# Optimization experiments

Measured on AMD Instinct MI355X. Metric: run time of the kernel, lower is better.

Reference implementation:

```python
import jax, jax.numpy as jnp
import numpy as np

N, M = 8192, 1024  # n_frames, feature dim (input_size == output_size == 1024)
Q_SCALE = 0.06
DROP_P = 0.5


def setup_inputs() -> dict:
    key = jax.random.key(0)
    kx, kk, kq, kv, ko, ku = jax.random.split(key, 6)
    w_std = 0.02
    return {
        "x": jax.random.normal(kx, (N, M), dtype=jnp.float32),
        # nn.Linear stores weight as [out_features, in_features]
        "Wk": jax.random.normal(kk, (M, M), dtype=jnp.float32) * w_std,
        "Wq": jax.random.normal(kq, (M, M), dtype=jnp.float32) * w_std,
        "Wv": jax.random.normal(kv, (M, M), dtype=jnp.float32) * w_std,
        "Wo": jax.random.normal(ko, (M, M), dtype=jnp.float32) * w_std,
        # uniform noise for dropout mask on the [N, N] attention matrix
        "u": jax.random.uniform(ku, (N, N), dtype=jnp.float32),
    }


def reference(x, Wk, Wq, Wv, Wo, u):
    # projections (bias-free Linear: y = x @ W.T)
    K = x @ Wk.T                      # [N, M]
    Q = (x @ Wq.T) * Q_SCALE          # [N, M], Q *= 0.06
    V = x @ Wv.T                      # [N, M]
    logits = Q @ K.T                  # [N, N]
    attn = jax.nn.softmax(logits, axis=-1)
    # Dropout(p=0.5) in train mode: keep with prob 0.5, scale by 1/(1-p)=2
    keep = jnp.where(u >= DROP_P, jnp.float32(1.0 / (1.0 - DROP_P)), jnp.float32(0.0))
    w = attn * keep                   # [N, N]
    y = w @ V                         # [N, M]
    return y @ Wo.T                   # [N, M]
```

## Files before the change

kernel.cpp:

```cpp
#include <hip/hip_runtime.h>
#include <cstdint>
#include <cstddef>

#define NFRAMES 8192
#define MDIM    1024
#define Q_SCALE 0.06f

#define BK 64
#define BM2 256
#define BN2 256
#define BM 256
#define BN 128

typedef __bf16 bf16x8 __attribute__((ext_vector_type(8)));
typedef float  f32x4  __attribute__((ext_vector_type(4)));
typedef unsigned short us8 __attribute__((ext_vector_type(8)));

__device__ __forceinline__ unsigned short f2bf(float f) {
  union { float f; uint32_t u; } a; a.f = f;
  uint32_t u = a.u;
  u += 0x7FFFu + ((u >> 16) & 1u);
  return (unsigned short)(u >> 16);
}
__device__ __forceinline__ float bf2f(unsigned short h) {
  union { uint32_t u; float f; } a; a.u = ((uint32_t)h) << 16; return a.f;
}

__device__ __forceinline__ void async_ld16(const void* g, void* l) {
  __builtin_amdgcn_global_load_lds(
      (const __attribute__((address_space(1))) void*)(uintptr_t)g,
      (__attribute__((address_space(3))) void*)(uint32_t)(uintptr_t)l,
      16, 0, 0);
}

__device__ __forceinline__ void store_val(float* p, float v) { *p = v; }
__device__ __forceinline__ void store_val(unsigned short* p, float v) { *p = f2bf(v); }

template <typename OutT>
__global__ __launch_bounds__(512, 2) void gemm_8ph(
    const unsigned short* __restrict__ A, int lda,
    const unsigned short* __restrict__ B, int ldb,
    OutT* __restrict__ C, int ldc, long cz, int kChunk)
{
  __shared__ alignas(16) unsigned short As[2 * BM2 * BK];
  __shared__ alignas(16) unsigned short Bs[2 * BN2 * BK];

  const int tid  = threadIdx.x;
  const int wave = tid >> 6;
  const int lane = tid & 63;

  const int gX  = (int)gridDim.x;
  const int nwg = gX * (int)gridDim.y;
  int bx = (int)blockIdx.x, by = (int)blockIdx.y;
  if ((nwg & 7) == 0) {
    const int L  = by * gX + bx;
    const int qq = nwg >> 3;
    const int Ls = (L & 7) * qq + (L >> 3);
    bx = Ls % gX; by = Ls / gX;
  }

  const int m0 = by * BM2, n0 = bx * BN2;
  const int wm = (wave >> 2) * 128;
  const int wn = (wave & 3) * 64;
  const int fr = lane & 15, fq = lane >> 4;

  const int kOff = (int)blockIdx.z * kChunk;
  OutT* Cz = C + (size_t)blockIdx.z * cz;

  const int l8 = lane >> 3, l7 = lane & 7;
  const size_t ldaB = (size_t)lda * 2, ldbB = (size_t)ldb * 2;
  const char* aSrc = (const char*)A + (size_t)(m0 + wave * 8 + l8) * ldaB
                     + (size_t)kOff * 2 + ((l7 ^ l8) << 4);
  const char* bSrc = (const char*)B + (size_t)(n0 + wave * 8 + l8) * ldbB
                     + (size_t)kOff * 2 + ((l7 ^ l8) << 4);

  const int xorv = (fr & 7) << 4;
  const int c0 = (fq * 16) ^ xorv;
  const int c1 = (64 + fq * 16) ^ xorv;
  const char* aRd = (const char*)As + (wm + fr) * 128;
  const char* bRd = (const char*)Bs + (wn + fr) * 128;
  const char* aB0 = aRd;
  const char* aB1 = aRd + 32768;
  const char* bB0 = bRd;
  const char* bB1 = bRd + 32768;

  f32x4 acc[8][4] = {};
  const int NT = kChunk >> 6;
  const int NI = NT >> 1;

#define SA(b, h, t) do { \
  async_ld16(aSrc + (size_t)((h) * 128)      * ldaB + (size_t)(t) * 128, \
             As + (b) * 16384 + (h) * 8192 + wave * 512); \
  async_ld16(aSrc + (size_t)((h) * 128 + 64) * ldaB + (size_t)(t) * 128, \
             As + (b) * 16384 + (h) * 8192 + 4096 + wave * 512); \
} while (0)
#define SB(b, h, t) do { \
  async_ld16(bSrc + (size_t)((h) * 128)      * ldbB + (size_t)(t) * 128, \
             Bs + (b) * 16384 + (h) * 8192 + wave * 512); \
  async_ld16(bSrc + (size_t)((h) * 128 + 64) * ldbB + (size_t)(t) * 128, \
             Bs + (b) * 16384 + (h) * 8192 + 4096 + wave * 512); \
} while (0)

#define RD_A(dst, base, mh) do { \
  _Pragma("unroll") \
  for (int m_ = 0; m_ < 4; ++m_) { \
    dst[m_][0] = *(const bf16x8*)((base) + ((mh) * 4 + m_) * 2048 + c0); \
    dst[m_][1] = *(const bf16x8*)((base) + ((mh) * 4 + m_) * 2048 + c1); \
  } \
} while (0)
#define RD_B(dst, base, nh) do { \
  _Pragma("unroll") \
  for (int n_ = 0; n_ < 2; ++n_) { \
    dst[n_][0] = *(const bf16x8*)((base) + ((nh) * 2 + n_) * 2048 + c0); \
    dst[n_][1] = *(const bf16x8*)((base) + ((nh) * 2 + n_) * 2048 + c1); \
  } \
} while (0)

#define BARR() __builtin_amdgcn_s_barrier()
#define LGKM0() do { asm volatile("s_waitcnt lgkmcnt(0)" ::: "memory"); \
                     __builtin_amdgcn_sched_barrier(0); } while (0)
#define MM(mh, nh, af, bf) do { \
  __builtin_amdgcn_s_setprio(1); \
  _Pragma("unroll") \
  for (int kk_ = 0; kk_ < 2; ++kk_) \
  _Pragma("unroll") \
  for (int m_ = 0; m_ < 4; ++m_) \
  _Pragma("unroll") \
  for (int n_ = 0; n_ < 2; ++n_) \
    acc[(mh) * 4 + m_][(nh) * 2 + n_] = __builtin_amdgcn_mfma_f32_16x16x32_bf16( \
        af[m_][kk_], bf[n_][kk_], acc[(mh) * 4 + m_][(nh) * 2 + n_], 0, 0, 0); \
  __builtin_amdgcn_s_setprio(0); \
} while (0)

#define BODY(G, T1) do { \
  bf16x8 aF[4][2], bF0[2][2], bF1[2][2]; \
   \
  RD_A(aF, aB0, 0); RD_B(bF0, bB0, 0); \
  SA(1, 0, (T1)); \
  BARR(); LGKM0(); MM(0, 0, aF, bF0); BARR(); \
   \
  RD_B(bF1, bB0, 1); \
  SA(1, 1, (T1)); \
  BARR(); LGKM0(); MM(0, 1, aF, bF1); BARR(); \
   \
  RD_A(aF, aB0, 1); \
  if (G) SB(0, 0, (T1) + 1); \
  BARR(); LGKM0(); MM(1, 0, aF, bF0); BARR(); \
   \
  if (G) SB(0, 1, (T1) + 1); \
  BARR(); MM(1, 1, aF, bF1); \
  if (G) { asm volatile("s_waitcnt vmcnt(4)" ::: "memory"); } \
  else   { asm volatile("s_waitcnt vmcnt(0)" ::: "memory"); } \
  BARR(); __builtin_amdgcn_sched_barrier(0); \
   \
  RD_A(aF, aB1, 0); RD_B(bF0, bB1, 0); \
  if (G) SA(0, 0, (T1) + 1); \
  BARR(); LGKM0(); MM(0, 0, aF, bF0); BARR(); \
   \
  RD_B(bF1, bB1, 1); \
  if (G) SA(0, 1, (T1) + 1); \
  BARR(); LGKM0(); MM(0, 1, aF, bF1); BARR(); \
   \
  RD_A(aF, aB1, 1); \
  if (G) SB(1, 0, (T1) + 2); \
  BARR(); LGKM0(); MM(1, 0, aF, bF0); BARR(); \
   \
  if (G) SB(1, 1, (T1) + 2); \
  BARR(); MM(1, 1, aF, bF1); \
  if (G) { asm volatile("s_waitcnt vmcnt(4)" ::: "memory"); } \
  BARR(); __builtin_amdgcn_sched_barrier(0); \
} while (0)

  SA(0, 0, 0); SA(0, 1, 0);
  SB(0, 0, 0); SB(0, 1, 0);
  SB(1, 0, 1); SB(1, 1, 1);
  asm volatile("s_waitcnt vmcnt(4)" ::: "memory");
  BARR();
  __builtin_amdgcn_sched_barrier(0);

  for (int i = 0; i + 1 < NI; ++i) {
    BODY(true, 2 * i + 1);
  }
  BODY(false, NT - 1);

#undef SA
#undef SB
#undef RD_A
#undef RD_B
#undef BARR
#undef LGKM0
#undef MM
#undef BODY

#pragma unroll
  for (int mf = 0; mf < 8; ++mf)
#pragma unroll
    for (int nf = 0; nf < 4; ++nf)
#pragma unroll
      for (int r = 0; r < 4; ++r) {
        int row = m0 + wm + mf * 16 + fq * 4 + r;
        int col = n0 + wn + nf * 16 + fr;
        store_val(&Cz[(size_t)row * ldc + col], acc[mf][nf][r]);
      }
}

template <typename OutT>
__global__ __launch_bounds__(512, 2) void gemm_bt8(
    const unsigned short* __restrict__ A, int lda,
    const unsigned short* __restrict__ B, int ldb,
    OutT* __restrict__ C, int ldc, int K)
{
  __shared__ alignas(16) unsigned short As[3 * BM * BK];
  __shared__ alignas(16) unsigned short Bs[3 * BN * BK];

  const int tid  = threadIdx.x;
  const int wave = tid >> 6;
  const int lane = tid & 63;

  const int gX  = (int)gridDim.x;
  const int nwg = gX * (int)gridDim.y;
  const int L   = (int)blockIdx.y * gX + (int)blockIdx.x;
  const int qq  = nwg >> 3;
  const int Ls  = (L & 7) * qq + (L >> 3);
  const int bx  = Ls % gX, by = Ls / gX;

  const int m0 = by * BM, n0 = bx * BN;
  const int wm = (wave >> 1) * 64;
  const int wn = (wave & 1) * 64;
  const int fr = lane & 15, fq = lane >> 4;

  const int l8 = lane >> 3, l7 = lane & 7;
  const size_t ldaB = (size_t)lda * 2, ldbB = (size_t)ldb * 2;
  const char* aSrc = (const char*)A + (size_t)(m0 + wave * 8 + l8) * ldaB + ((l7 ^ l8) << 4);
  const char* bSrc = (const char*)B + (size_t)(n0 + wave * 8 + l8) * ldbB + ((l7 ^ l8) << 4);
  unsigned short* aDst = As + wave * 512;
  unsigned short* bDst = Bs + wave * 512;

  const int xorv = (fr & 7) << 4;
  const int cA0 = (fq * 16) ^ xorv;
  const int cA1 = (64 + fq * 16) ^ xorv;
  const char* aRd = (const char*)As + (wm + fr) * 128;
  const char* bRd = (const char*)Bs + (wn + fr) * 128;

  f32x4 acc[4][4] = {};
  const int NT = K >> 6;

#define STA(buf, s, t) async_ld16(aSrc + (size_t)((s) * 64) * ldaB + (size_t)(t) * 128, \
                                  aDst + (buf) * 16384 + (s) * 4096)
#define STB(buf, s, t) async_ld16(bSrc + (size_t)((s) * 64) * ldbB + (size_t)(t) * 128, \
                                  bDst + (buf) * 8192 + (s) * 4096)

  STA(0, 0, 0); STA(0, 1, 0); STA(0, 2, 0); STA(0, 3, 0); STB(0, 0, 0); STB(0, 1, 0);
  if (NT > 1) { STA(1, 0, 1); STA(1, 1, 1); STA(1, 2, 1); STA(1, 3, 1); STB(1, 0, 1); STB(1, 1, 1); }
  asm volatile("s_waitcnt vmcnt(6)" ::: "memory");
  __builtin_amdgcn_s_barrier();

  for (int t = 0; t < NT; ++t) {
    const int cur = t % 3;
    const int u   = t + 2;
    const int ub  = u % 3;
    const bool st = (u < NT);
    const char* aB = aRd + cur * 32768;
    const char* bB = bRd + cur * 16384;

    bf16x8 bh[4][2];
#pragma unroll
    for (int j = 0; j < 4; ++j) {
      bh[j][0] = *(const bf16x8*)(bB + j * 2048 + cA0);
      bh[j][1] = *(const bf16x8*)(bB + j * 2048 + cA1);
    }
    bf16x8 a0[2][2];
#pragma unroll
    for (int i = 0; i < 2; ++i) {
      a0[i][0] = *(const bf16x8*)(aB + i * 2048 + cA0);
      a0[i][1] = *(const bf16x8*)(aB + i * 2048 + cA1);
    }
    if (st) { STA(ub, 0, u); STA(ub, 1, u); STB(ub, 0, u); }
    __builtin_amdgcn_s_barrier();
    asm volatile("s_waitcnt lgkmcnt(0)" ::: "memory");
    __builtin_amdgcn_sched_barrier(0);
    __builtin_amdgcn_s_setprio(1);
#pragma unroll
    for (int kk = 0; kk < 2; ++kk)
#pragma unroll
      for (int i = 0; i < 2; ++i)
#pragma unroll
        for (int j = 0; j < 4; ++j)
          acc[i][j] = __builtin_amdgcn_mfma_f32_16x16x32_bf16(
              kk ? a0[i][1] : a0[i][0], kk ? bh[j][1] : bh[j][0], acc[i][j], 0, 0, 0);
    __builtin_amdgcn_s_setprio(0);
    __builtin_amdgcn_s_barrier();

    bf16x8 a1[2][2];
#pragma unroll
    for (int i = 0; i < 2; ++i) {
      a1[i][0] = *(const bf16x8*)(aB + (2 + i) * 2048 + cA0);
      a1[i][1] = *(const bf16x8*)(aB + (2 + i) * 2048 + cA1);
    }
    if (st) { STA(ub, 2, u); STA(ub, 3, u); STB(ub, 1, u); }
    if (st) { asm volatile("s_waitcnt vmcnt(6)" ::: "memory"); }
    else    { asm volatile("s_waitcnt vmcnt(0)" ::: "memory"); }
    __builtin_amdgcn_s_barrier();
    asm volatile("s_waitcnt lgkmcnt(0)" ::: "memory");
    __builtin_amdgcn_sched_barrier(0);
    __builtin_amdgcn_s_setprio(1);
#pragma unroll
    for (int kk = 0; kk < 2; ++kk)
#pragma unroll
      for (int i = 0; i < 2; ++i)
#pragma unroll
        for (int j = 0; j < 4; ++j)
          acc[2 + i][j] = __builtin_amdgcn_mfma_f32_16x16x32_bf16(
              kk ? a1[i][1] : a1[i][0], kk ? bh[j][1] : bh[j][0], acc[2 + i][j], 0, 0, 0);
    __builtin_amdgcn_s_setprio(0);
    __builtin_amdgcn_s_barrier();
  }
#undef STA
#undef STB

#pragma unroll
  for (int i = 0; i < 4; ++i)
#pragma unroll
    for (int j = 0; j < 4; ++j)
#pragma unroll
      for (int r = 0; r < 4; ++r) {
        int row = m0 + wm + i * 16 + fq * 4 + r;
        int col = n0 + wn + j * 16 + fr;
        store_val(&C[(size_t)row * ldc + col], acc[i][j][r]);
      }
}

__global__ __launch_bounds__(256) void softmax_dropout_kernel(
    const unsigned short* __restrict__ S, const float* __restrict__ U,
    unsigned short* __restrict__ P)
{
  const int row = blockIdx.x;
  const us8*   s8 = (const us8*)(S + (size_t)row * NFRAMES);
  const f32x4* u4 = (const f32x4*)(U + (size_t)row * NFRAMES);
  us8*         p8 = (us8*)(P + (size_t)row * NFRAMES);
  const int tid = threadIdx.x;
  const int lane = tid & 63, wave = tid >> 6;

  float v[32];
  float mx = -3.4e38f;
#pragma unroll
  for (int j = 0; j < 4; ++j) {
    us8 t = __builtin_nontemporal_load(s8 + j * 256 + tid);
#pragma unroll
    for (int e = 0; e < 8; ++e) {
      float f = bf2f(t[e]);
      v[j * 8 + e] = f;
      mx = fmaxf(mx, f);
    }
  }
#pragma unroll
  for (int o = 32; o > 0; o >>= 1) mx = fmaxf(mx, __shfl_xor(mx, o));
  __shared__ float redm[4];
  __shared__ float reds[4];
  if (lane == 0) redm[wave] = mx;
  __syncthreads();
  mx = fmaxf(fmaxf(redm[0], redm[1]), fmaxf(redm[2], redm[3]));

  float sum = 0.f;
#pragma unroll
  for (int i = 0; i < 32; ++i) { v[i] = __expf(v[i] - mx); sum += v[i]; }
#pragma unroll
  for (int o = 32; o > 0; o >>= 1) sum += __shfl_xor(sum, o);
  if (lane == 0) reds[wave] = sum;
  __syncthreads();
  sum = reds[0] + reds[1] + reds[2] + reds[3];
  float inv = 1.0f / sum;

#pragma unroll
  for (int j = 0; j < 4; ++j) {
    f32x4 ua = __builtin_nontemporal_load(u4 + (j * 256 + tid) * 2);
    f32x4 ub = __builtin_nontemporal_load(u4 + (j * 256 + tid) * 2 + 1);
    us8 o;
    o[0] = f2bf(v[j*8+0] * inv * (ua[0] >= 0.5f ? 2.0f : 0.0f));
    o[1] = f2bf(v[j*8+1] * inv * (ua[1] >= 0.5f ? 2.0f : 0.0f));
    o[2] = f2bf(v[j*8+2] * inv * (ua[2] >= 0.5f ? 2.0f : 0.0f));
    o[3] = f2bf(v[j*8+3] * inv * (ua[3] >= 0.5f ? 2.0f : 0.0f));
    o[4] = f2bf(v[j*8+4] * inv * (ub[0] >= 0.5f ? 2.0f : 0.0f));
    o[5] = f2bf(v[j*8+5] * inv * (ub[1] >= 0.5f ? 2.0f : 0.0f));
    o[6] = f2bf(v[j*8+6] * inv * (ub[2] >= 0.5f ? 2.0f : 0.0f));
    o[7] = f2bf(v[j*8+7] * inv * (ub[3] >= 0.5f ? 2.0f : 0.0f));
    p8[j * 256 + tid] = o;
  }
}

__device__ __forceinline__ void cvt4(const float* in, unsigned short* out, int i, float s) {
  float4 t = ((const float4*)in)[i];
  ushort4 o;
  o.x = f2bf(t.x * s); o.y = f2bf(t.y * s); o.z = f2bf(t.z * s); o.w = f2bf(t.w * s);
  ((ushort4*)out)[i] = o;
}

__global__ __launch_bounds__(256) void cvt_all(
    const float* __restrict__ x, const float* __restrict__ Wk,
    const float* __restrict__ Wq, const float* __restrict__ Wv,
    const float* __restrict__ Wo,
    unsigned short* __restrict__ xb, unsigned short* __restrict__ wkq,
    unsigned short* __restrict__ wvb, unsigned short* __restrict__ wob)
{
  int i = blockIdx.x * 256 + threadIdx.x;
  const int XSZ = (NFRAMES * MDIM) / 4;
  const int WSZ = (MDIM * MDIM) / 4;
  if (i < XSZ) { cvt4(x, xb, i, 1.0f); return; }
  i -= XSZ;
  if (i < WSZ) { cvt4(Wk, wkq, i, 1.0f); return; }
  i -= WSZ;
  if (i < WSZ) { cvt4(Wq, wkq + MDIM * MDIM, i, Q_SCALE); return; }
  i -= WSZ;
  if (i < WSZ) { cvt4(Wv, wvb, i, 1.0f); return; }
  i -= WSZ;
  if (i < WSZ) { cvt4(Wo, wob, i, 1.0f); return; }
}

__global__ __launch_bounds__(256) void reduce2_bf16(
    const float* __restrict__ Yp, long zs,
    unsigned short* __restrict__ out, int n4)
{
  int i = blockIdx.x * 256 + threadIdx.x;
  if (i < n4) {
    f32x4 a = __builtin_nontemporal_load((const f32x4*)Yp + i);
    f32x4 b = __builtin_nontemporal_load((const f32x4*)(Yp + zs) + i);
    ushort4 o;
    o.x = f2bf(a[0] + b[0]);
    o.y = f2bf(a[1] + b[1]);
    o.z = f2bf(a[2] + b[2]);
    o.w = f2bf(a[3] + b[3]);
    ((ushort4*)out)[i] = o;
  }
}

extern "C" void kernel_launch(void* const* d_in, const int* in_sizes, int n_in,
                              void* d_out, int out_size, void* d_ws, size_t ws_size,
                              hipStream_t stream) {
  const float* x  = (const float*)d_in[0];
  const float* Wk = (const float*)d_in[1];
  const float* Wq = (const float*)d_in[2];
  const float* Wv = (const float*)d_in[3];
  const float* Wo = (const float*)d_in[4];
  const float* u  = (const float*)d_in[5];
  float* out = (float*)d_out;

  const int N = NFRAMES, M = MDIM;
  char* base = (char*)d_ws;
  size_t off = 0;
  auto alloc = [&](size_t bytes) -> void* {
    void* p = base + off; off += (bytes + 255) & ~(size_t)255; return p;
  };
  unsigned short* xb  = (unsigned short*)alloc((size_t)N * M * 2);
  unsigned short* wkq = (unsigned short*)alloc((size_t)2 * M * M * 2);
  unsigned short* wvb = (unsigned short*)alloc((size_t)M * M * 2);
  unsigned short* wob = (unsigned short*)alloc((size_t)M * M * 2);
  unsigned short* KQb = (unsigned short*)alloc((size_t)N * 2 * M * 2);
  unsigned short* Vt  = (unsigned short*)alloc((size_t)M * N * 2);
  unsigned short* yb  = (unsigned short*)alloc((size_t)N * M * 2);

  size_t avail = ws_size > off ? ws_size - off : 0;
  int R = 256;
  const int cands[6] = {8192, 4096, 2048, 1024, 512, 256};
  for (int ci = 0; ci < 6; ++ci) {
    size_t need = (size_t)cands[ci] * N * 2 * 2 + 1024;
    if (need <= avail) { R = cands[ci]; break; }
  }
  unsigned short* Sb = (unsigned short*)alloc((size_t)R * N * 2);
  unsigned short* Pb = (unsigned short*)alloc((size_t)R * N * 2);
  float* Yp = (float*)Sb;

  {
    int total4 = (N * M + 4 * M * M) / 4;
    cvt_all<<<(total4 + 255) / 256, 256, 0, stream>>>(x, Wk, Wq, Wv, Wo, xb, wkq, wvb, wob);
  }

  gemm_8ph<unsigned short><<<dim3(2 * M / BN2, N / BM2), 512, 0, stream>>>(
      xb, M, wkq, M, KQb, 2 * M, 0, M);
  gemm_bt8<unsigned short><<<dim3(N / BN, M / BM), 512, 0, stream>>>(
      wvb, M, xb, M, Vt, N, M);

  for (int i0 = 0; i0 < N; i0 += R) {
    gemm_8ph<unsigned short><<<dim3(N / BN2, R / BM2), 512, 0, stream>>>(
        KQb + M + (size_t)i0 * 2 * M, 2 * M,
        KQb, 2 * M,
        Sb, N, 0, M);
    softmax_dropout_kernel<<<R, 256, 0, stream>>>(Sb, u + (size_t)i0 * N, Pb);
    gemm_8ph<float><<<dim3(M / BN2, R / BM2, 2), 512, 0, stream>>>(
        Pb, N, Vt, N, Yp, M, (long)R * M, N / 2);
    reduce2_bf16<<<(R * M / 4 + 255) / 256, 256, 0, stream>>>(
        Yp, (long)R * M, yb + (size_t)i0 * M, R * M / 4);
  }

  gemm_bt8<float><<<dim3(M / BN, N / BM), 512, 0, stream>>>(
      yb, M, wob, M, out, M, M);
}
```

Baseline: 722.4 us.

## Fold output projection into value weights and drop lgkmcnt waits

Precomputes W2 = Wo·Wv as a 1024x1024 GEMM, then forms Zt = (x·W2ᵀ)ᵀ directly, so the attention-weighted sum writes the final output and the trailing N×M×M output-projection GEMM plus the bf16 y buffer go away. The split-K reduce now writes float output directly. Separately, it removes the explicit lgkmcnt(0) waits and sched_barriers in both GEMM kernels and leaves the compiler to place LDS waits, and it guards the block swizzle for grids not divisible by 8. The combined W2 product is rounded to bf16, which changes numerics slightly, and the Wv transpose in cvt_all uses strided 2-byte stores.

Measured after the change: 722.8 us. No clear change (+0.1%).

```diff
diff --git a/kernel.cpp b/kernel.cpp
--- a/kernel.cpp
+++ b/kernel.cpp
@@ -117,8 +117,6 @@
 } while (0)
 
 #define BARR() __builtin_amdgcn_s_barrier()
-#define LGKM0() do { asm volatile("s_waitcnt lgkmcnt(0)" ::: "memory"); \
-                     __builtin_amdgcn_sched_barrier(0); } while (0)
 #define MM(mh, nh, af, bf) do { \
   __builtin_amdgcn_s_setprio(1); \
   _Pragma("unroll") \
@@ -137,38 +135,38 @@
    \
   RD_A(aF, aB0, 0); RD_B(bF0, bB0, 0); \
   SA(1, 0, (T1)); \
-  BARR(); LGKM0(); MM(0, 0, aF, bF0); BARR(); \
+  BARR(); MM(0, 0, aF, bF0); BARR(); \
    \
   RD_B(bF1, bB0, 1); \
   SA(1, 1, (T1)); \
-  BARR(); LGKM0(); MM(0, 1, aF, bF1); BARR(); \
+  BARR(); MM(0, 1, aF, bF1); BARR(); \
    \
   RD_A(aF, aB0, 1); \
   if (G) SB(0, 0, (T1) + 1); \
-  BARR(); LGKM0(); MM(1, 0, aF, bF0); BARR(); \
+  BARR(); MM(1, 0, aF, bF0); BARR(); \
    \
   if (G) SB(0, 1, (T1) + 1); \
   BARR(); MM(1, 1, aF, bF1); \
   if (G) { asm volatile("s_waitcnt vmcnt(4)" ::: "memory"); } \
   else   { asm volatile("s_waitcnt vmcnt(0)" ::: "memory"); } \
-  BARR(); __builtin_amdgcn_sched_barrier(0); \
+  BARR(); \
    \
   RD_A(aF, aB1, 0); RD_B(bF0, bB1, 0); \
   if (G) SA(0, 0, (T1) + 1); \
-  BARR(); LGKM0(); MM(0, 0, aF, bF0); BARR(); \
+  BARR(); MM(0, 0, aF, bF0); BARR(); \
    \
   RD_B(bF1, bB1, 1); \
   if (G) SA(0, 1, (T1) + 1); \
-  BARR(); LGKM0(); MM(0, 1, aF, bF1); BARR(); \
+  BARR(); MM(0, 1, aF, bF1); BARR(); \
    \
   RD_A(aF, aB1, 1); \
   if (G) SB(1, 0, (T1) + 2); \
-  BARR(); LGKM0(); MM(1, 0, aF, bF0); BARR(); \
+  BARR(); MM(1, 0, aF, bF0); BARR(); \
    \
   if (G) SB(1, 1, (T1) + 2); \
   BARR(); MM(1, 1, aF, bF1); \
   if (G) { asm volatile("s_waitcnt vmcnt(4)" ::: "memory"); } \
-  BARR(); __builtin_amdgcn_sched_barrier(0); \
+  BARR(); \
 } while (0)
 
   SA(0, 0, 0); SA(0, 1, 0);
@@ -176,7 +174,6 @@
   SB(1, 0, 1); SB(1, 1, 1);
   asm volatile("s_waitcnt vmcnt(4)" ::: "memory");
   BARR();
-  __builtin_amdgcn_sched_barrier(0);
 
   for (int i = 0; i + 1 < NI; ++i) {
     BODY(true, 2 * i + 1);
@@ -188,7 +185,6 @@
 #undef RD_A
 #undef RD_B
 #undef BARR
-#undef LGKM0
 #undef MM
 #undef BODY
 
@@ -219,10 +215,13 @@
 
   const int gX  = (int)gridDim.x;
   const int nwg = gX * (int)gridDim.y;
-  const int L   = (int)blockIdx.y * gX + (int)blockIdx.x;
-  const int qq  = nwg >> 3;
-  const int Ls  = (L & 7) * qq + (L >> 3);
-  const int bx  = Ls % gX, by = Ls / gX;
+  int bx = (int)blockIdx.x, by = (int)blockIdx.y;
+  if ((nwg & 7) == 0) {
+    const int L  = by * gX + bx;
+    const int qq = nwg >> 3;
+    const int Ls = (L & 7) * qq + (L >> 3);
+    bx = Ls % gX; by = Ls / gX;
+  }
 
   const int m0 = by * BM, n0 = bx * BN;
   const int wm = (wave >> 1) * 64;
@@ -277,8 +276,6 @@
     }
     if (st) { STA(ub, 0, u); STA(ub, 1, u); STB(ub, 0, u); }
     __builtin_amdgcn_s_barrier();
-    asm volatile("s_waitcnt lgkmcnt(0)" ::: "memory");
-    __builtin_amdgcn_sched_barrier(0);
     __builtin_amdgcn_s_setprio(1);
 #pragma unroll
     for (int kk = 0; kk < 2; ++kk)
@@ -301,8 +298,6 @@
     if (st) { asm volatile("s_waitcnt vmcnt(6)" ::: "memory"); }
     else    { asm volatile("s_waitcnt vmcnt(0)" ::: "memory"); }
     __builtin_amdgcn_s_barrier();
-    asm volatile("s_waitcnt lgkmcnt(0)" ::: "memory");
-    __builtin_amdgcn_sched_barrier(0);
     __builtin_amdgcn_s_setprio(1);
 #pragma unroll
     for (int kk = 0; kk < 2; ++kk)
@@ -400,7 +395,7 @@
     const float* __restrict__ Wq, const float* __restrict__ Wv,
     const float* __restrict__ Wo,
     unsigned short* __restrict__ xb, unsigned short* __restrict__ wkq,
-    unsigned short* __restrict__ wvb, unsigned short* __restrict__ wob)
+    unsigned short* __restrict__ wvT, unsigned short* __restrict__ wob)
 {
   int i = blockIdx.x * 256 + threadIdx.x;
   const int XSZ = (NFRAMES * MDIM) / 4;
@@ -411,25 +406,34 @@
   i -= WSZ;
   if (i < WSZ) { cvt4(Wq, wkq + MDIM * MDIM, i, Q_SCALE); return; }
   i -= WSZ;
-  if (i < WSZ) { cvt4(Wv, wvb, i, 1.0f); return; }
+  if (i < WSZ) {
+    float4 t = ((const float4*)Wv)[i];
+    int lin = i * 4;
+    int m = lin >> 10, k = lin & 1023;
+    wvT[(size_t)(k + 0) * MDIM + m] = f2bf(t.x);
+    wvT[(size_t)(k + 1) * MDIM + m] = f2bf(t.y);
+    wvT[(size_t)(k + 2) * MDIM + m] = f2bf(t.z);
+    wvT[(size_t)(k + 3) * MDIM + m] = f2bf(t.w);
+    return;
+  }
   i -= WSZ;
   if (i < WSZ) { cvt4(Wo, wob, i, 1.0f); return; }
 }
 
-__global__ __launch_bounds__(256) void reduce2_bf16(
+__global__ __launch_bounds__(256) void reduce2_f32(
     const float* __restrict__ Yp, long zs,
-    unsigned short* __restrict__ out, int n4)
+    float* __restrict__ out, int n4)
 {
   int i = blockIdx.x * 256 + threadIdx.x;
   if (i < n4) {
     f32x4 a = __builtin_nontemporal_load((const f32x4*)Yp + i);
     f32x4 b = __builtin_nontemporal_load((const f32x4*)(Yp + zs) + i);
-    ushort4 o;
-    o.x = f2bf(a[0] + b[0]);
-    o.y = f2bf(a[1] + b[1]);
-    o.z = f2bf(a[2] + b[2]);
-    o.w = f2bf(a[3] + b[3]);
-    ((ushort4*)out)[i] = o;
+    f32x4 o;
+    o[0] = a[0] + b[0];
+    o[1] = a[1] + b[1];
+    o[2] = a[2] + b[2];
+    o[3] = a[3] + b[3];
+    ((f32x4*)out)[i] = o;
   }
 }
 
@@ -452,11 +456,11 @@
   };
   unsigned short* xb  = (unsigned short*)alloc((size_t)N * M * 2);
   unsigned short* wkq = (unsigned short*)alloc((size_t)2 * M * M * 2);
-  unsigned short* wvb = (unsigned short*)alloc((size_t)M * M * 2);
+  unsigned short* wvT = (unsigned short*)alloc((size_t)M * M * 2);
   unsigned short* wob = (unsigned short*)alloc((size_t)M * M * 2);
+  unsigned short* w2b = (unsigned short*)alloc((size_t)M * M * 2);
   unsigned short* KQb = (unsigned short*)alloc((size_t)N * 2 * M * 2);
-  unsigned short* Vt  = (unsigned short*)alloc((size_t)M * N * 2);
-  unsigned short* yb  = (unsigned short*)alloc((size_t)N * M * 2);
+  unsigned short* Zt  = (unsigned short*)alloc((size_t)M * N * 2);
 
   size_t avail = ws_size > off ? ws_size - off : 0;
   int R = 256;
@@ -471,13 +475,17 @@
 
   {
     int total4 = (N * M + 4 * M * M) / 4;
-    cvt_all<<<(total4 + 255) / 256, 256, 0, stream>>>(x, Wk, Wq, Wv, Wo, xb, wkq, wvb, wob);
-  }
+    cvt_all<<<(total4 + 255) / 256, 256, 0, stream>>>(x, Wk, Wq, Wv, Wo, xb, wkq, wvT, wob);
+  }
+
+  gemm_bt8<unsigned short><<<dim3(M / BN, M / BM), 512, 0, stream>>>(
+      wob, M, wvT, M, w2b, M, M);
 
   gemm_8ph<unsigned short><<<dim3(2 * M / BN2, N / BM2), 512, 0, stream>>>(
       xb, M, wkq, M, KQb, 2 * M, 0, M);
+
   gemm_bt8<unsigned short><<<dim3(N / BN, M / BM), 512, 0, stream>>>(
-      wvb, M, xb, M, Vt, N, M);
+      w2b, M, xb, M, Zt, N, M);
 
   for (int i0 = 0; i0 < N; i0 += R) {
     gemm_8ph<unsigned short><<<dim3(N / BN2, R / BM2), 512, 0, stream>>>(
@@ -486,11 +494,8 @@
         Sb, N, 0, M);
     softmax_dropout_kernel<<<R, 256, 0, stream>>>(Sb, u + (size_t)i0 * N, Pb);
     gemm_8ph<float><<<dim3(M / BN2, R / BM2, 2), 512, 0, stream>>>(
-        Pb, N, Vt, N, Yp, M, (long)R * M, N / 2);
-    reduce2_bf16<<<(R * M / 4 + 255) / 256, 256, 0, stream>>>(
-        Yp, (long)R * M, yb + (size_t)i0 * M, R * M / 4);
-  }
-
-  gemm_bt8<float><<<dim3(M / BN, N / BM), 512, 0, stream>>>(
-      yb, M, wob, M, out, M, M);
-}
+        Pb, N, Zt, N, Yp, M, (long)R * M, N / 2);
+    reduce2_f32<<<(R * M / 4 + 255) / 256, 256, 0, stream>>>(
+        Yp, (long)R * M, out + (size_t)i0 * M, R * M / 4);
+  }
+}
```
